# Kernel optimization log

Measured on AMD Instinct MI355X. Metric: run time of the kernel, lower is better.

## Reference

```python
import jax, jax.numpy as jnp
import numpy as np

ROUTING_ITERS = 3
EPS = 1e-07


def setup_inputs() -> dict:
    key = jax.random.key(0)
    k1, k2 = jax.random.split(key)
    B, IN_CAPS, OUT_CAPS, POSE = 128, 2048, 32, 4
    votes = jax.random.normal(k1, (B, IN_CAPS, OUT_CAPS, POSE), dtype=jnp.float32)
    activations_in = jax.random.uniform(k2, (B, IN_CAPS), dtype=jnp.float32)
    return {"votes": votes, "activations_in": activations_in}


def _safe_norm(s, axis=-1):
    # NOTE: original safe_norm always keeps dims (reduce_sum keepdims=True, then sqrt)
    return jnp.sqrt(jnp.sum(jnp.square(s), axis=axis, keepdims=True) + EPS)


def _squash(s):
    s_norm = _safe_norm(s, axis=-1)                 # [..., 1]
    scale = jnp.square(s_norm) / (1.0 + jnp.square(s_norm))
    return scale * (s / s_norm)


def reference(votes, activations_in):
    # votes: [B, in_caps, out_caps, pose]
    B, in_caps, out_caps, _ = votes.shape
    b_ij = jnp.zeros((B, in_caps, out_caps), dtype=jnp.float32)
    v_j = None
    for _ in range(ROUTING_ITERS):
        c_ij = jax.nn.softmax(b_ij, axis=2)                       # [B, I, O]
        s_j = jnp.einsum('bio,biop->bop', c_ij, votes)            # [B, O, P]
        v_j = _squash(s_j)                                        # [B, O, P]
        v_stop = jax.lax.stop_gradient(v_j)
        agreement = jnp.einsum('biop,bop->bio', votes, v_stop)    # [B, I, O]
        b_ij = b_ij + agreement
    poses_out = v_j                                               # [B, O, P]
    activations_out = _safe_norm(poses_out, axis=-1)              # [B, O, 1] (keepdims bug preserved)
    return poses_out, activations_out
```

## Files before the change

### kernel.cpp

```cpp
#include <hip/hip_runtime.h>


#define BATCH 128
#define IC 2048
#define OC 32
#define POSE 4
#define REPS 1e-7f

#define CHUNKS 16
#define CHUNK_I (IC / CHUNKS)
#define BLOCK_T 256
#define GROUPS (BLOCK_T / 32)
#define IPT (CHUNK_I / GROUPS)
#define ILP 4
#define STEPS (IPT / ILP)

#define PART_IDX(t, b, c, o) ((((size_t)(t) * BATCH + (b)) * CHUNKS + (c)) * OC + (o))

__device__ __forceinline__ float dot4(const float4 a, const float4 b) {
    return a.x*b.x + a.y*b.y + a.z*b.z + a.w*b.w;
}

__device__ __forceinline__ float4 squash4(const float4 s) {
    const float n2 = s.x*s.x + s.y*s.y + s.z*s.z + s.w*s.w + REPS;
    const float f = n2 / (1.f + n2) * rsqrtf(n2);
    return make_float4(f*s.x, f*s.y, f*s.z, f*s.w);
}

__device__ __forceinline__ float4 reduce_squash(
    const float4* __restrict__ partials, int t, int b, int o, float scale)
{
    float4 acc = make_float4(0.f, 0.f, 0.f, 0.f);
    #pragma unroll
    for (int c = 0; c < CHUNKS; ++c) {
        const float4 p = partials[PART_IDX(t, b, c, o)];
        acc.x += p.x; acc.y += p.y; acc.z += p.z; acc.w += p.w;
    }
    acc.x *= scale; acc.y *= scale; acc.z *= scale; acc.w *= scale;
    return squash4(acc);
}

__device__ __forceinline__ void block_reduce_store(
    float4 s_acc, float4* lds_s, float4* __restrict__ partials,
    int t, int b, int chunk, int g, int o)
{
    lds_s[g * 32 + o] = s_acc;
    __syncthreads();
    if (threadIdx.x < 32) {
        float4 tot = lds_s[o];
        #pragma unroll
        for (int gg = 1; gg < GROUPS; ++gg) {
            const float4 x = lds_s[gg * 32 + o];
            tot.x += x.x; tot.y += x.y; tot.z += x.z; tot.w += x.w;
        }
        partials[PART_IDX(t, b, chunk, o)] = tot;
    }
}

__device__ __forceinline__ void accum4f(const float4 v0, const float4 v1,
                                        const float4 v2, const float4 v3,
                                        const float4 vh, float4& s_acc)
{
    const float l0 = dot4(v0, vh);
    const float l1 = dot4(v1, vh);
    const float l2 = dot4(v2, vh);
    const float l3 = dot4(v3, vh);
    float e0 = __expf(l0), e1 = __expf(l1), e2 = __expf(l2), e3 = __expf(l3);
    float t0 = e0, t1 = e1, t2 = e2, t3 = e3;
    #pragma unroll
    for (int d = 16; d >= 1; d >>= 1) {
        t0 += __shfl_xor(t0, d);
        t1 += __shfl_xor(t1, d);
        t2 += __shfl_xor(t2, d);
        t3 += __shfl_xor(t3, d);
    }
    const float c0 = e0 * __builtin_amdgcn_rcpf(t0);
    const float c1 = e1 * __builtin_amdgcn_rcpf(t1);
    const float c2 = e2 * __builtin_amdgcn_rcpf(t2);
    const float c3 = e3 * __builtin_amdgcn_rcpf(t3);

    s_acc.x += c0*v0.x + c1*v1.x + c2*v2.x + c3*v3.x;
    s_acc.y += c0*v0.y + c1*v1.y + c2*v2.y + c3*v3.y;
    s_acc.z += c0*v0.z + c1*v1.z + c2*v2.z + c3*v3.z;
    s_acc.w += c0*v0.w + c1*v1.w + c2*v2.w + c3*v3.w;
}

__global__ __launch_bounds__(BLOCK_T) void routing_t0(
    const float4* __restrict__ votes,
    float4* __restrict__ partials)
{
    const int b     = blockIdx.x >> 4;
    const int chunk = blockIdx.x & (CHUNKS - 1);
    const int o     = threadIdx.x & 31;
    const int g     = threadIdx.x >> 5;

    __shared__ float4 lds_s[GROUPS * 32];

    const float4* vb = votes + ((size_t)b * IC + (size_t)chunk * CHUNK_I) * OC;

    float4 s0 = make_float4(0.f, 0.f, 0.f, 0.f);
    #pragma unroll
    for (int s = 0; s < IPT; ++s) {
        const float4 v = vb[(size_t)(s * GROUPS + g) * OC + o];
        s0.x += v.x; s0.y += v.y; s0.z += v.z; s0.w += v.w;
    }
    block_reduce_store(s0, lds_s, partials, 0, b, chunk, g, o);
}

template <int T>
__global__ __launch_bounds__(BLOCK_T) void routing_pass(
    const float4* __restrict__ votes,
    float4* __restrict__ partials)
{
    const int b     = blockIdx.x >> 4;
    const int chunk = blockIdx.x & (CHUNKS - 1);
    const int o     = threadIdx.x & 31;
    const int g     = threadIdx.x >> 5;

    __shared__ float4 lds_s[GROUPS * 32];
    __shared__ float4 vh_s[32];

    if (threadIdx.x < 32) {
        float4 vh = reduce_squash(partials, 0, b, o, 1.f / 32.f);
        if (T == 2) {
            const float4 v1 = reduce_squash(partials, 1, b, o, 1.f);
            vh.x += v1.x; vh.y += v1.y; vh.z += v1.z; vh.w += v1.w;
        }
        vh_s[o] = vh;
    }
    __syncthreads();
    const float4 vh = vh_s[o];

    const float4* vb = votes + ((size_t)b * IC + (size_t)chunk * CHUNK_I) * OC;

    float4 s_acc = make_float4(0.f, 0.f, 0.f, 0.f);
    #pragma unroll
    for (int st = 0; st < STEPS; ++st) {
        const int base = st * (ILP * GROUPS) + g;
        const float4 v0 = vb[(size_t)(base + 0 * GROUPS) * OC + o];
        const float4 v1 = vb[(size_t)(base + 1 * GROUPS) * OC + o];
        const float4 v2 = vb[(size_t)(base + 2 * GROUPS) * OC + o];
        const float4 v3 = vb[(size_t)(base + 3 * GROUPS) * OC + o];
        accum4f(v0, v1, v2, v3, vh, s_acc);
    }
    block_reduce_store(s_acc, lds_s, partials, T, b, chunk, g, o);
}

__global__ __launch_bounds__(256) void routing_finalize(
    const float4* __restrict__ partials,
    float* __restrict__ out)
{
    const int idx = blockIdx.x * blockDim.x + threadIdx.x;
    if (idx >= BATCH * OC) return;
    const int b = idx >> 5, o = idx & 31;
    const float4 v = reduce_squash(partials, 2, b, o, 1.f);
    ((float4*)out)[idx] = v;
    const float a = sqrtf(v.x*v.x + v.y*v.y + v.z*v.z + v.w*v.w + REPS);
    out[BATCH * OC * POSE + idx] = a;
}

extern "C" void kernel_launch(void* const* d_in, const int* in_sizes, int n_in,
                              void* d_out, int out_size, void* d_ws, size_t ws_size,
                              hipStream_t stream) {
    const float4* votes = (const float4*)d_in[0];

    float4* partials = (float4*)d_ws;

    routing_t0<<<BATCH * CHUNKS, BLOCK_T, 0, stream>>>(votes, partials);
    routing_pass<1><<<BATCH * CHUNKS, BLOCK_T, 0, stream>>>(votes, partials);
    routing_pass<2><<<BATCH * CHUNKS, BLOCK_T, 0, stream>>>(votes, partials);
    routing_finalize<<<(BATCH * OC + 255) / 256, 256, 0, stream>>>(
        partials, (float*)d_out);
}
```

Before: 236.1 us.

## Cache votes as fp16 in thread-ordered workspace for later routing passes

The first pass now reads the fp32 votes with nontemporal loads, sums them, and also writes an fp16 copy to workspace, laid out in exact per-thread access order. The two later routing passes read this half-size copy instead of the fp32 votes, which halves their memory traffic. The cost is an extra 64 MB write in the first pass and fp16 rounding of the votes, which changes numerical accuracy. An extra barrier was added before the block reduction.

```diff
diff --git a/kernel.cpp b/kernel.cpp
--- a/kernel.cpp
+++ b/kernel.cpp
@@ -1,4 +1,5 @@
 #include <hip/hip_runtime.h>
+#include <hip/hip_fp16.h>
 
 
 #define BATCH 128
@@ -6,16 +7,30 @@
 #define OC 32
 #define POSE 4
 #define REPS 1e-7f
-
 #define CHUNKS 16
 #define CHUNK_I (IC / CHUNKS)
 #define BLOCK_T 256
 #define GROUPS (BLOCK_T / 32)
-#define IPT (CHUNK_I / GROUPS)
 #define ILP 4
-#define STEPS (IPT / ILP)
+#define STEPS (CHUNK_I / (GROUPS * ILP))
 
 #define PART_IDX(t, b, c, o) ((((size_t)(t) * BATCH + (b)) * CHUNKS + (c)) * OC + (o))
+
+typedef float        f32x4 __attribute__((ext_vector_type(4)));
+typedef unsigned int u32x4 __attribute__((ext_vector_type(4)));
+
+__device__ __forceinline__ unsigned packh2(const float a, const float b) {
+    union { __half2 h; unsigned u; } c;
+    c.h = __float22half2_rn(make_float2(a, b));
+    return c.u;
+}
+__device__ __forceinline__ float4 unpackh2(const unsigned lo, const unsigned hi) {
+    union { unsigned u; __half2 h; } a, b;
+    a.u = lo; b.u = hi;
+    const float2 f0 = __half22float2(a.h);
+    const float2 f1 = __half22float2(b.h);
+    return make_float4(f0.x, f0.y, f1.x, f1.y);
+}
 
 __device__ __forceinline__ float dot4(const float4 a, const float4 b) {
     return a.x*b.x + a.y*b.y + a.z*b.z + a.w*b.w;
@@ -57,63 +72,57 @@
     }
 }
 
-__device__ __forceinline__ void accum4f(const float4 v0, const float4 v1,
-                                        const float4 v2, const float4 v3,
-                                        const float4 vh, float4& s_acc)
-{
-    const float l0 = dot4(v0, vh);
-    const float l1 = dot4(v1, vh);
-    const float l2 = dot4(v2, vh);
-    const float l3 = dot4(v3, vh);
-    float e0 = __expf(l0), e1 = __expf(l1), e2 = __expf(l2), e3 = __expf(l3);
-    float t0 = e0, t1 = e1, t2 = e2, t3 = e3;
-    #pragma unroll
-    for (int d = 16; d >= 1; d >>= 1) {
-        t0 += __shfl_xor(t0, d);
-        t1 += __shfl_xor(t1, d);
-        t2 += __shfl_xor(t2, d);
-        t3 += __shfl_xor(t3, d);
-    }
-    const float c0 = e0 * __builtin_amdgcn_rcpf(t0);
-    const float c1 = e1 * __builtin_amdgcn_rcpf(t1);
-    const float c2 = e2 * __builtin_amdgcn_rcpf(t2);
-    const float c3 = e3 * __builtin_amdgcn_rcpf(t3);
-
-    s_acc.x += c0*v0.x + c1*v1.x + c2*v2.x + c3*v3.x;
-    s_acc.y += c0*v0.y + c1*v1.y + c2*v2.y + c3*v3.y;
-    s_acc.z += c0*v0.z + c1*v1.z + c2*v2.z + c3*v3.z;
-    s_acc.w += c0*v0.w + c1*v1.w + c2*v2.w + c3*v3.w;
-}
-
 __global__ __launch_bounds__(BLOCK_T) void routing_t0(
-    const float4* __restrict__ votes,
+    const f32x4* __restrict__ votes,
+    u32x4* __restrict__ v16,
     float4* __restrict__ partials)
 {
-    const int b     = blockIdx.x >> 4;
-    const int chunk = blockIdx.x & (CHUNKS - 1);
+    const int blk   = blockIdx.x;
+    const int b     = blk >> 4;
+    const int chunk = blk & (CHUNKS - 1);
     const int o     = threadIdx.x & 31;
     const int g     = threadIdx.x >> 5;
 
     __shared__ float4 lds_s[GROUPS * 32];
 
-    const float4* vb = votes + ((size_t)b * IC + (size_t)chunk * CHUNK_I) * OC;
-
-    float4 s0 = make_float4(0.f, 0.f, 0.f, 0.f);
+    float4 s_acc = make_float4(0.f, 0.f, 0.f, 0.f);
+    const f32x4* vb = votes + (size_t)b * IC * OC;
+    const int i0 = chunk * CHUNK_I;
+
     #pragma unroll
-    for (int s = 0; s < IPT; ++s) {
-        const float4 v = vb[(size_t)(s * GROUPS + g) * OC + o];
-        s0.x += v.x; s0.y += v.y; s0.z += v.z; s0.w += v.w;
-    }
-    block_reduce_store(s0, lds_s, partials, 0, b, chunk, g, o);
+    for (int step = 0; step < STEPS; ++step) {
+        const int ia = i0 + step * (GROUPS * ILP) + g;
+        const f32x4 n0 = __builtin_nontemporal_load(&vb[(size_t)(ia + 0 * GROUPS) * OC + o]);
+        const f32x4 n1 = __builtin_nontemporal_load(&vb[(size_t)(ia + 1 * GROUPS) * OC + o]);
+        const f32x4 n2 = __builtin_nontemporal_load(&vb[(size_t)(ia + 2 * GROUPS) * OC + o]);
+        const f32x4 n3 = __builtin_nontemporal_load(&vb[(size_t)(ia + 3 * GROUPS) * OC + o]);
+
+        s_acc.x += (n0.x + n1.x) + (n2.x + n3.x);
+        s_acc.y += (n0.y + n1.y) + (n2.y + n3.y);
+        s_acc.z += (n0.z + n1.z) + (n2.z + n3.z);
+        s_acc.w += (n0.w + n1.w) + (n2.w + n3.w);
+
+        u32x4 lo, hi;
+        lo.x = packh2(n0.x, n0.y); lo.y = packh2(n0.z, n0.w);
+        lo.z = packh2(n1.x, n1.y); lo.w = packh2(n1.z, n1.w);
+        hi.x = packh2(n2.x, n2.y); hi.y = packh2(n2.z, n2.w);
+        hi.z = packh2(n3.x, n3.y); hi.w = packh2(n3.z, n3.w);
+        const size_t slot = ((size_t)(blk * STEPS + step) * BLOCK_T + threadIdx.x) * 2;
+        __builtin_nontemporal_store(lo, &v16[slot + 0]);
+        __builtin_nontemporal_store(hi, &v16[slot + 1]);
+    }
+
+    block_reduce_store(s_acc, lds_s, partials, 0, b, chunk, g, o);
 }
 
 template <int T>
 __global__ __launch_bounds__(BLOCK_T) void routing_pass(
-    const float4* __restrict__ votes,
+    const u32x4* __restrict__ v16,
     float4* __restrict__ partials)
 {
-    const int b     = blockIdx.x >> 4;
-    const int chunk = blockIdx.x & (CHUNKS - 1);
+    const int blk   = blockIdx.x;
+    const int b     = blk >> 4;
+    const int chunk = blk & (CHUNKS - 1);
     const int o     = threadIdx.x & 31;
     const int g     = threadIdx.x >> 5;
 
@@ -131,18 +140,42 @@
     __syncthreads();
     const float4 vh = vh_s[o];
 
-    const float4* vb = votes + ((size_t)b * IC + (size_t)chunk * CHUNK_I) * OC;
-
     float4 s_acc = make_float4(0.f, 0.f, 0.f, 0.f);
     #pragma unroll
-    for (int st = 0; st < STEPS; ++st) {
-        const int base = st * (ILP * GROUPS) + g;
-        const float4 v0 = vb[(size_t)(base + 0 * GROUPS) * OC + o];
-        const float4 v1 = vb[(size_t)(base + 1 * GROUPS) * OC + o];
-        const float4 v2 = vb[(size_t)(base + 2 * GROUPS) * OC + o];
-        const float4 v3 = vb[(size_t)(base + 3 * GROUPS) * OC + o];
-        accum4f(v0, v1, v2, v3, vh, s_acc);
-    }
+    for (int step = 0; step < STEPS; ++step) {
+        const size_t slot = ((size_t)(blk * STEPS + step) * BLOCK_T + threadIdx.x) * 2;
+        const u32x4 lo = v16[slot + 0];
+        const u32x4 hi = v16[slot + 1];
+        const float4 v0 = unpackh2(lo.x, lo.y);
+        const float4 v1 = unpackh2(lo.z, lo.w);
+        const float4 v2 = unpackh2(hi.x, hi.y);
+        const float4 v3 = unpackh2(hi.z, hi.w);
+
+        const float l0 = dot4(v0, vh);
+        const float l1 = dot4(v1, vh);
+        const float l2 = dot4(v2, vh);
+        const float l3 = dot4(v3, vh);
+        float e0 = __expf(l0), e1 = __expf(l1), e2 = __expf(l2), e3 = __expf(l3);
+        float t0 = e0, t1 = e1, t2 = e2, t3 = e3;
+        #pragma unroll
+        for (int d = 16; d >= 1; d >>= 1) {
+            t0 += __shfl_xor(t0, d);
+            t1 += __shfl_xor(t1, d);
+            t2 += __shfl_xor(t2, d);
+            t3 += __shfl_xor(t3, d);
+        }
+        const float c0 = e0 * __builtin_amdgcn_rcpf(t0);
+        const float c1 = e1 * __builtin_amdgcn_rcpf(t1);
+        const float c2 = e2 * __builtin_amdgcn_rcpf(t2);
+        const float c3 = e3 * __builtin_amdgcn_rcpf(t3);
+
+        s_acc.x += c0*v0.x + c1*v1.x + c2*v2.x + c3*v3.x;
+        s_acc.y += c0*v0.y + c1*v1.y + c2*v2.y + c3*v3.y;
+        s_acc.z += c0*v0.z + c1*v1.z + c2*v2.z + c3*v3.z;
+        s_acc.w += c0*v0.w + c1*v1.w + c2*v2.w + c3*v3.w;
+    }
+
+    __syncthreads();
     block_reduce_store(s_acc, lds_s, partials, T, b, chunk, g, o);
 }
 
@@ -162,13 +195,14 @@
 extern "C" void kernel_launch(void* const* d_in, const int* in_sizes, int n_in,
                               void* d_out, int out_size, void* d_ws, size_t ws_size,
                               hipStream_t stream) {
-    const float4* votes = (const float4*)d_in[0];
+    const f32x4* votes = (const f32x4*)d_in[0];
 
     float4* partials = (float4*)d_ws;
-
-    routing_t0<<<BATCH * CHUNKS, BLOCK_T, 0, stream>>>(votes, partials);
-    routing_pass<1><<<BATCH * CHUNKS, BLOCK_T, 0, stream>>>(votes, partials);
-    routing_pass<2><<<BATCH * CHUNKS, BLOCK_T, 0, stream>>>(votes, partials);
+    u32x4*  v16      = (u32x4*)((char*)d_ws + (size_t)4 * 1024 * 1024);
+
+    routing_t0<<<BATCH * CHUNKS, BLOCK_T, 0, stream>>>(votes, v16, partials);
+    routing_pass<1><<<BATCH * CHUNKS, BLOCK_T, 0, stream>>>(v16, partials);
+    routing_pass<2><<<BATCH * CHUNKS, BLOCK_T, 0, stream>>>(v16, partials);
     routing_finalize<<<(BATCH * OC + 255) / 256, 256, 0, stream>>>(
         partials, (float*)d_out);
 }
```

Result: slower. 245.6 us (+4.1%).
